# Performance work log

Measured on AMD Instinct MI355X. Metric: run time of the kernel, lower is better.

The kernel has to match this reference:

```python
import jax, jax.numpy as jnp
import numpy as np

NUM_BAGS = 16384
IN_DIM = 768
# deterministic ragged bag sizes 1..16 (avg 8.5) -> total = 1024 * 136 = 139264
_SIZES = (np.arange(NUM_BAGS) % 16) + 1
TOTAL = int(_SIZES.sum())  # 139264


def setup_inputs() -> dict:
    key = jax.random.key(0)
    k1, k2 = jax.random.split(key)
    scope = jnp.asarray(np.cumsum(_SIZES).astype(np.int32))  # cumulative end offsets, last == TOTAL
    x = jax.random.normal(k1, (TOTAL, IN_DIM), dtype=jnp.float32)
    attn_w = jax.random.normal(k2, (IN_DIM,), dtype=jnp.float32) * 0.01  # init.normal_(std=0.01)
    return {"x": x, "attn_w": attn_w, "scope": scope}


def reference(x, attn_w, scope):
    # x: [total, d], scope: [num_bags] cumulative end offsets (int32)
    total = x.shape[0]
    scale = IN_DIM ** -0.5
    # segment id for each row: index of first scope entry > row index
    seg_ids = jnp.searchsorted(scope, jnp.arange(total), side='right')
    logits = scale * (x @ attn_w)  # [total]
    # segmented, numerically-stable softmax over each bag
    seg_max = jax.ops.segment_max(logits, seg_ids, num_segments=NUM_BAGS)
    e = jnp.exp(logits - seg_max[seg_ids])
    denom = jax.ops.segment_sum(e, seg_ids, num_segments=NUM_BAGS)
    attn = e / denom[seg_ids]  # [total], per-bag softmax weights
    # weighted sum pooling per bag: [num_bags, d]
    bag_logits = jax.ops.segment_sum(attn[:, None] * x, seg_ids, num_segments=NUM_BAGS)
    return bag_logits, attn
```

## Files before the change

### kernel.cpp

```cpp
#include <hip/hip_runtime.h>
#include <math.h>

#define NUM_BAGS 16384
#define IN_DIM   768
#define MAX_BAG  16
#define WPB      2

typedef float v4f __attribute__((ext_vector_type(4)));

__global__ __launch_bounds__(128) void BagAttention_27092653703393_kernel(
    const float* __restrict__ x,
    const float* __restrict__ attn_w,
    const int*   __restrict__ scope,
    float* __restrict__ bag_out,
    float* __restrict__ attn_out)
{
    const int t    = threadIdx.x;
    const int lane = t & 63;
    const int wave = t >> 6;
    const int b    = blockIdx.x * WPB + wave;

    const int end_off   = scope[b];
    const int start_off = (b == 0) ? 0 : scope[b - 1];
    const int n         = end_off - start_off;

    const v4f* w4 = reinterpret_cast<const v4f*>(attn_w);
    const v4f w0 = w4[lane];
    const v4f w1 = w4[64 + lane];
    const v4f w2 = w4[128 + lane];

    const float scale = 0.03608439182435161f;

    float s = 0.f;
    v4f a0 = (v4f)(0.f);
    v4f a1 = (v4f)(0.f);
    v4f a2 = (v4f)(0.f);
    float myatt_e = 0.f;

    const v4f* xr = reinterpret_cast<const v4f*>(x + (size_t)start_off * IN_DIM);

#pragma unroll
    for (int i = 0; i < MAX_BAG; ++i) {
        if (i < n) {
            const v4f* row = xr + i * (IN_DIM / 4);
            const v4f x0 = __builtin_nontemporal_load(row + lane);
            const v4f x1 = __builtin_nontemporal_load(row + 64 + lane);
            const v4f x2 = __builtin_nontemporal_load(row + 128 + lane);

            const v4f m0 = x0 * w0;
            const v4f m1 = x1 * w1;
            const v4f m2 = x2 * w2;
            float p0 = m0[0] + m0[1] + m0[2] + m0[3];
            float p1 = m1[0] + m1[1] + m1[2] + m1[3];
            float p2 = m2[0] + m2[1] + m2[2] + m2[3];
            float p = (p0 + p1) + p2;
#pragma unroll
            for (int off = 32; off; off >>= 1) p += __shfl_xor(p, off);

            const float e = __expf(p * scale);
            s += e;
            if (lane == i) myatt_e = e;
            a0 += x0 * e;
            a1 += x1 * e;
            a2 += x2 * e;
        }
    }

    const float inv = 1.f / s;

    if (lane < n) {
        __builtin_nontemporal_store(myatt_e * inv, attn_out + start_off + lane);
    }

    a0 *= inv;
    a1 *= inv;
    a2 *= inv;

    v4f* out4 = reinterpret_cast<v4f*>(bag_out + (size_t)b * IN_DIM);
    __builtin_nontemporal_store(a0, out4 + lane);
    __builtin_nontemporal_store(a1, out4 + 64 + lane);
    __builtin_nontemporal_store(a2, out4 + 128 + lane);
}

extern "C" void kernel_launch(void* const* d_in, const int* in_sizes, int n_in,
                              void* d_out, int out_size, void* d_ws, size_t ws_size,
                              hipStream_t stream) {
    const float* x      = (const float*)d_in[0];
    const float* attn_w = (const float*)d_in[1];
    const int*   scope  = (const int*)d_in[2];

    float* out      = (float*)d_out;
    float* bag_out  = out;
    float* attn_out = out + (size_t)NUM_BAGS * IN_DIM;

    BagAttention_27092653703393_kernel<<<NUM_BAGS / WPB, 128, 0, stream>>>(
        x, attn_w, scope, bag_out, attn_out);
}
```

Before: 110.8 us.

## Split each bag across two waves with row prefetch and LDS reduction

Each bag is now processed by two waves that take alternating rows, with a software-prefetched next row in a dynamic loop, and partial sums combined through shared memory before normalization and output. This aims to increase memory-level parallelism and wave occupancy for a bandwidth-bound ragged reduction. It adds a block barrier, LDS traffic and a redundant final prefetch, and drops the non-temporal hints on loads.

```diff
diff --git a/kernel.cpp b/kernel.cpp
--- a/kernel.cpp
+++ b/kernel.cpp
@@ -3,22 +3,26 @@
 
 #define NUM_BAGS 16384
 #define IN_DIM   768
-#define MAX_BAG  16
-#define WPB      2
+#define BAGS_PER_BLOCK 2
 
 typedef float v4f __attribute__((ext_vector_type(4)));
 
-__global__ __launch_bounds__(128) void BagAttention_27092653703393_kernel(
+__global__ __launch_bounds__(256) void BagAttention_27092653703393_kernel(
     const float* __restrict__ x,
     const float* __restrict__ attn_w,
     const int*   __restrict__ scope,
     float* __restrict__ bag_out,
     float* __restrict__ attn_out)
 {
+    __shared__ float sh_a[BAGS_PER_BLOCK][12][64];
+    __shared__ float sh_s[BAGS_PER_BLOCK][2];
+
     const int t    = threadIdx.x;
     const int lane = t & 63;
     const int wave = t >> 6;
-    const int b    = blockIdx.x * WPB + wave;
+    const int bib  = wave >> 1;
+    const int h    = wave & 1;
+    const int b    = blockIdx.x * BAGS_PER_BLOCK + bib;
 
     const int end_off   = scope[b];
     const int start_off = (b == 0) ? 0 : scope[b - 1];
@@ -32,54 +36,64 @@
     const float scale = 0.03608439182435161f;
 
     float s = 0.f;
-    v4f a0 = (v4f)(0.f);
-    v4f a1 = (v4f)(0.f);
-    v4f a2 = (v4f)(0.f);
-    float myatt_e = 0.f;
+    v4f a0 = (v4f)(0.f), a1 = (v4f)(0.f), a2 = (v4f)(0.f);
+    float my_e = 0.f;
 
-    const v4f* xr = reinterpret_cast<const v4f*>(x + (size_t)start_off * IN_DIM);
+    const int cnt = (n - h + 1) >> 1;
+    const v4f* rp = reinterpret_cast<const v4f*>(x + (size_t)(start_off + h) * IN_DIM);
+    const int RSTRIDE = 2 * (IN_DIM / 4);
 
-#pragma unroll
-    for (int i = 0; i < MAX_BAG; ++i) {
-        if (i < n) {
-            const v4f* row = xr + i * (IN_DIM / 4);
-            const v4f x0 = __builtin_nontemporal_load(row + lane);
-            const v4f x1 = __builtin_nontemporal_load(row + 64 + lane);
-            const v4f x2 = __builtin_nontemporal_load(row + 128 + lane);
+    if (cnt > 0) {
+        v4f c0 = rp[lane], c1 = rp[64 + lane], c2 = rp[128 + lane];
+        for (int j = 0; j < cnt; ++j) {
+            const int jn = (j + 1 < cnt) ? (j + 1) : j;
+            const v4f* np = rp + jn * RSTRIDE;
+            const v4f n0 = np[lane], n1 = np[64 + lane], n2 = np[128 + lane];
 
-            const v4f m0 = x0 * w0;
-            const v4f m1 = x1 * w1;
-            const v4f m2 = x2 * w2;
-            float p0 = m0[0] + m0[1] + m0[2] + m0[3];
-            float p1 = m1[0] + m1[1] + m1[2] + m1[3];
-            float p2 = m2[0] + m2[1] + m2[2] + m2[3];
-            float p = (p0 + p1) + p2;
+            const v4f m0 = c0 * w0, m1 = c1 * w1, m2 = c2 * w2;
+            float p = (m0[0] + m0[1] + m0[2] + m0[3])
+                    + (m1[0] + m1[1] + m1[2] + m1[3])
+                    + (m2[0] + m2[1] + m2[2] + m2[3]);
 #pragma unroll
             for (int off = 32; off; off >>= 1) p += __shfl_xor(p, off);
 
             const float e = __expf(p * scale);
             s += e;
-            if (lane == i) myatt_e = e;
-            a0 += x0 * e;
-            a1 += x1 * e;
-            a2 += x2 * e;
+            if (lane == j) my_e = e;
+            a0 += c0 * e;  a1 += c1 * e;  a2 += c2 * e;
+            c0 = n0; c1 = n1; c2 = n2;
         }
     }
 
-    const float inv = 1.f / s;
+    if (h == 0) {
+#pragma unroll
+        for (int k = 0; k < 4; ++k) sh_a[bib][k][lane]     = a0[k];
+#pragma unroll
+        for (int k = 0; k < 4; ++k) sh_a[bib][4 + k][lane] = a1[k];
+#pragma unroll
+        for (int k = 0; k < 4; ++k) sh_a[bib][8 + k][lane] = a2[k];
+    }
+    if (lane == 0) sh_s[bib][h] = s;
+    __syncthreads();
 
-    if (lane < n) {
-        __builtin_nontemporal_store(myatt_e * inv, attn_out + start_off + lane);
+    const float inv = 1.f / (sh_s[bib][0] + sh_s[bib][1]);
+
+    const int r = h + 2 * lane;
+    if (r < n) __builtin_nontemporal_store(my_e * inv, attn_out + start_off + r);
+
+    if (h == 1) {
+#pragma unroll
+        for (int k = 0; k < 4; ++k) a0[k] += sh_a[bib][k][lane];
+#pragma unroll
+        for (int k = 0; k < 4; ++k) a1[k] += sh_a[bib][4 + k][lane];
+#pragma unroll
+        for (int k = 0; k < 4; ++k) a2[k] += sh_a[bib][8 + k][lane];
+        a0 *= inv; a1 *= inv; a2 *= inv;
+        v4f* out4 = reinterpret_cast<v4f*>(bag_out + (size_t)b * IN_DIM);
+        __builtin_nontemporal_store(a0, out4 + lane);
+        __builtin_nontemporal_store(a1, out4 + 64 + lane);
+        __builtin_nontemporal_store(a2, out4 + 128 + lane);
     }
-
-    a0 *= inv;
-    a1 *= inv;
-    a2 *= inv;
-
-    v4f* out4 = reinterpret_cast<v4f*>(bag_out + (size_t)b * IN_DIM);
-    __builtin_nontemporal_store(a0, out4 + lane);
-    __builtin_nontemporal_store(a1, out4 + 64 + lane);
-    __builtin_nontemporal_store(a2, out4 + 128 + lane);
 }
 
 extern "C" void kernel_launch(void* const* d_in, const int* in_sizes, int n_in,
@@ -93,6 +107,6 @@
     float* bag_out  = out;
     float* attn_out = out + (size_t)NUM_BAGS * IN_DIM;
 
-    BagAttention_27092653703393_kernel<<<NUM_BAGS / WPB, 128, 0, stream>>>(
+    BagAttention_27092653703393_kernel<<<NUM_BAGS / BAGS_PER_BLOCK, 256, 0, stream>>>(
         x, attn_w, scope, bag_out, attn_out);
 }
```

Result: no change. 112.5 us (+1.5%).
